# Performance work log

Measured on AMD Instinct MI355X. Metric: run time of the kernel, lower is better.

The kernel has to match this reference:

```python
import jax, jax.numpy as jnp
import numpy as np

EMBED_DIM = 1024
NUM_HEADS = 16
HEAD_DIM = EMBED_DIM // NUM_HEADS
ROPE_BASE = 10000.0


def _rope_cos_sin(seq_len, dim, dtype=jnp.float32):
    inv_freq = 1.0 / (ROPE_BASE ** (jnp.arange(0, dim, 2, dtype=jnp.float32) / dim))
    pos = jnp.arange(seq_len, dtype=jnp.float32)
    freqs = jnp.outer(pos, inv_freq)              # [S, dim/2]
    emb = jnp.concatenate([freqs, freqs], axis=-1)  # [S, dim]
    return jnp.cos(emb).astype(dtype), jnp.sin(emb).astype(dtype)


def _rotate_half(x):
    half = x.shape[-1] // 2
    return jnp.concatenate([-x[..., half:], x[..., :half]], axis=-1)


def setup_inputs() -> dict:
    key = jax.random.key(0)
    ks = jax.random.split(key, 12)
    B, S, E = 4, 2048, EMBED_DIM
    std = 1.0 / np.sqrt(E)
    inp = {
        'query': jax.random.normal(ks[0], (B, S, E), jnp.float32),
        'key': jax.random.normal(ks[1], (B, S, E), jnp.float32),
        'value': jax.random.normal(ks[2], (B, S, E), jnp.float32),
        'Wq': jax.random.uniform(ks[3], (E, E), jnp.float32, -std, std),
        'bq': jax.random.uniform(ks[4], (E,), jnp.float32, -std, std),
        'Wk': jax.random.uniform(ks[5], (E, E), jnp.float32, -std, std),
        'bk': jax.random.uniform(ks[6], (E,), jnp.float32, -std, std),
        'Wv': jax.random.uniform(ks[7], (E, E), jnp.float32, -std, std),
        'bv': jax.random.uniform(ks[8], (E,), jnp.float32, -std, std),
        'Wo': jax.random.uniform(ks[9], (E, E), jnp.float32, -std, std),
        'bo': jax.random.uniform(ks[10], (E,), jnp.float32, -std, std),
    }
    return inp


def reference(query, key, value, Wq, bq, Wk, bk, Wv, bv, Wo, bo):
    B, Sq, E = query.shape
    Sk = key.shape[1]
    H, D = NUM_HEADS, HEAD_DIM
    scale = D ** -0.5

    q = query @ Wq.T + bq
    k = key @ Wk.T + bk
    v = value @ Wv.T + bv

    # [B, H, S, D]
    q = q.reshape(B, Sq, H, D).transpose(0, 2, 1, 3)
    k = k.reshape(B, Sk, H, D).transpose(0, 2, 1, 3)
    v = v.reshape(B, Sk, H, D).transpose(0, 2, 1, 3)

    cos, sin = _rope_cos_sin(Sq, D, q.dtype)  # [S, D]; module slices by seq_len_q for both
    cos = cos[None, None]  # [1,1,S,D]
    sin = sin[None, None]
    q = q * cos + _rotate_half(q) * sin
    k = k * cos + _rotate_half(k) * sin

    scores = jnp.einsum('bhqd,bhkd->bhqk', q, k) * scale
    attn = jax.nn.softmax(scores, axis=-1)  # dropout p=0.0 -> identity
    out = jnp.einsum('bhqk,bhkd->bhqd', attn, v)
    out = out.transpose(0, 2, 1, 3).reshape(B, Sq, E)
    out = out @ Wo.T + bo
    attn_avg = attn.mean(axis=1)  # [B, Sq, Sk]
    return out, attn_avg
```

## Files before the change

kernel.cpp:

```cpp
#include <hip/hip_runtime.h>
#include <math.h>

#define TB 4
#define TS 2048
#define TE 1024
#define TH 16
#define TD 64
#define TM_ (TB*TS)

#define WS_Q   0
#define WS_K   8388608
#define WS_L   16777216
#define WS_TAB 16908288

typedef __attribute__((ext_vector_type(8))) short bf16x8;
typedef __attribute__((ext_vector_type(4))) float f32x4;

static __device__ inline unsigned fbits(float x) {
    union { float f; unsigned u; } v; v.f = x; return v.u;
}
static __device__ inline float bits2f(unsigned u) {
    union { unsigned u; float f; } v; v.u = u; return v.f;
}
static __device__ inline unsigned pack_rhu(float a, float b) {
    return __builtin_amdgcn_perm(fbits(b) + 0x8000u, fbits(a) + 0x8000u, 0x07060302u);
}
static __device__ inline void split2(float x0, float x1, unsigned& hp, unsigned& lp) {
    unsigned u0 = fbits(x0) + 0x8000u, u1 = fbits(x1) + 0x8000u;
    hp = __builtin_amdgcn_perm(u1, u0, 0x07060302u);
    float h0 = bits2f(u0 & 0xffff0000u);
    float h1 = bits2f(u1 & 0xffff0000u);
    lp = pack_rhu(x0 - h0, x1 - h1);
}

template<int MODE>
__global__ __launch_bounds__(256, 2)
void gemm_nt(const float* __restrict__ X, const float* __restrict__ W,
             const float* __restrict__ bias, float* __restrict__ out)
{
    __shared__ short Ah[128][40], Al[128][40];
    __shared__ short Bh[128][40], Bl[128][40];

    const int tid  = threadIdx.x;
    const int lane = tid & 63;
    const int wv   = tid >> 6;
    const int t16  = lane & 15;
    const int quad = lane >> 4;
    const int wm   = (wv >> 1) * 64;
    const int wn   = (wv & 1) * 64;
    const int m0 = blockIdx.y * 128;
    const int n0 = blockIdx.x * 128;
    const int K = TE, N = TE;

    const int srow = tid >> 1;
    const int skc  = (tid & 1) * 16;
    const float* Xp = X + (size_t)(m0 + srow) * K + skc;
    const float* Wp = W + (size_t)(n0 + srow) * K + skc;

    f32x4 acc[4][4];
    #pragma unroll
    for (int i = 0; i < 4; ++i)
        #pragma unroll
        for (int j = 0; j < 4; ++j) acc[i][j] = (f32x4){0.f, 0.f, 0.f, 0.f};

    for (int kt = 0; kt < K; kt += 32) {
        __syncthreads();
        {
            const float* xp = Xp + kt;
            float4 x0 = *(const float4*)(xp);
            float4 x1 = *(const float4*)(xp + 4);
            float4 x2 = *(const float4*)(xp + 8);
            float4 x3 = *(const float4*)(xp + 12);
            const float* wp = Wp + kt;
            float4 w0 = *(const float4*)(wp);
            float4 w1 = *(const float4*)(wp + 4);
            float4 w2 = *(const float4*)(wp + 8);
            float4 w3 = *(const float4*)(wp + 12);

            unsigned H[8], L[8];
            split2(x0.x, x0.y, H[0], L[0]);
            split2(x0.z, x0.w, H[1], L[1]);
            split2(x1.x, x1.y, H[2], L[2]);
            split2(x1.z, x1.w, H[3], L[3]);
            split2(x2.x, x2.y, H[4], L[4]);
            split2(x2.z, x2.w, H[5], L[5]);
            split2(x3.x, x3.y, H[6], L[6]);
            split2(x3.z, x3.w, H[7], L[7]);
            *(uint4*)&Ah[srow][skc]     = make_uint4(H[0], H[1], H[2], H[3]);
            *(uint4*)&Ah[srow][skc + 8] = make_uint4(H[4], H[5], H[6], H[7]);
            *(uint4*)&Al[srow][skc]     = make_uint4(L[0], L[1], L[2], L[3]);
            *(uint4*)&Al[srow][skc + 8] = make_uint4(L[4], L[5], L[6], L[7]);

            split2(w0.x, w0.y, H[0], L[0]);
            split2(w0.z, w0.w, H[1], L[1]);
            split2(w1.x, w1.y, H[2], L[2]);
            split2(w1.z, w1.w, H[3], L[3]);
            split2(w2.x, w2.y, H[4], L[4]);
            split2(w2.z, w2.w, H[5], L[5]);
            split2(w3.x, w3.y, H[6], L[6]);
            split2(w3.z, w3.w, H[7], L[7]);
            *(uint4*)&Bh[srow][skc]     = make_uint4(H[0], H[1], H[2], H[3]);
            *(uint4*)&Bh[srow][skc + 8] = make_uint4(H[4], H[5], H[6], H[7]);
            *(uint4*)&Bl[srow][skc]     = make_uint4(L[0], L[1], L[2], L[3]);
            *(uint4*)&Bl[srow][skc + 8] = make_uint4(L[4], L[5], L[6], L[7]);
        }
        __syncthreads();

        bf16x8 ah[4], al[4], bh[4], bl[4];
        #pragma unroll
        for (int i = 0; i < 4; ++i) {
            ah[i] = *(const bf16x8*)&Ah[wm + i * 16 + t16][quad * 8];
            al[i] = *(const bf16x8*)&Al[wm + i * 16 + t16][quad * 8];
            bh[i] = *(const bf16x8*)&Bh[wn + i * 16 + t16][quad * 8];
            bl[i] = *(const bf16x8*)&Bl[wn + i * 16 + t16][quad * 8];
        }
        #pragma unroll
        for (int i = 0; i < 4; ++i)
            #pragma unroll
            for (int j = 0; j < 4; ++j) {
                acc[i][j] = __builtin_amdgcn_mfma_f32_16x16x32_bf16(ah[i], bh[j], acc[i][j], 0, 0, 0);
                acc[i][j] = __builtin_amdgcn_mfma_f32_16x16x32_bf16(al[i], bh[j], acc[i][j], 0, 0, 0);
                acc[i][j] = __builtin_amdgcn_mfma_f32_16x16x32_bf16(ah[i], bl[j], acc[i][j], 0, 0, 0);
            }
    }

    if (MODE == 2) {
        short* o16 = (short*)out;
        const int b = m0 >> 11;
        const int sbase0 = (m0 & 2047) + wm + quad * 4;
        #pragma unroll
        for (int j = 0; j < 4; ++j) {
            const int n = n0 + wn + j * 16 + t16;
            const int h = n >> 6, d = n & 63;
            const float bv = bias[n];
            const size_t base = ((size_t)(b * TH + h) * TD + d) * TS;
            #pragma unroll
            for (int i = 0; i < 4; ++i) {
                const int s = sbase0 + i * 16;
                uint2 p = make_uint2(pack_rhu(acc[i][j][0] + bv, acc[i][j][1] + bv),
                                     pack_rhu(acc[i][j][2] + bv, acc[i][j][3] + bv));
                *(uint2*)(o16 + base + s) = p;
            }
        }
        return;
    }

    #pragma unroll
    for (int j = 0; j < 4; ++j) {
        const int n = n0 + wn + j * 16 + t16;
        const float bv = bias[n];
        if (MODE == 0) {
            #pragma unroll
            for (int i = 0; i < 4; ++i)
                #pragma unroll
                for (int r = 0; r < 4; ++r) {
                    const int m = m0 + wm + i * 16 + quad * 4 + r;
                    out[(size_t)m * N + n] = acc[i][j][r] + bv;
                }
        } else {
            const int h = n >> 6, d = n & 63;
            #pragma unroll
            for (int i = 0; i < 4; ++i)
                #pragma unroll
                for (int r = 0; r < 4; ++r) {
                    const int m = m0 + wm + i * 16 + quad * 4 + r;
                    const int bb_ = m >> 11, s = m & 2047;
                    out[((size_t)(bb_ * TH + h) * TS + s) * TD + d] = acc[i][j][r] + bv;
                }
        }
    }
}

__global__ void rope_table(float* __restrict__ tab)
{
    const int idx = blockIdx.x * 256 + threadIdx.x;
    const int d = idx & 31, s = idx >> 5;
    const float e = (float)(2 * d) / 64.0f;
    const float inv = 1.0f / powf(10000.0f, e);
    const float a = (float)s * inv;
    tab[2 * idx + 0] = cosf(a);
    tab[2 * idx + 1] = sinf(a);
}

__global__ void rope_apply(float* __restrict__ Q, float* __restrict__ Kv,
                           const float* __restrict__ tab)
{
    const int idx = blockIdx.x * 256 + threadIdx.x;
    const int half = TB * TH * TS * 32;
    float* P = (idx < half) ? Q : Kv;
    const int u = idx & (half - 1);
    const int d = u & 31;
    const int s = (u >> 5) & 2047;
    const int bh = u >> 16;
    const size_t base = (size_t)bh * (TS * TD) + (size_t)s * TD;
    const float c  = tab[2 * (s * 32 + d) + 0];
    const float sn = tab[2 * (s * 32 + d) + 1];
    const float x0 = P[base + d], x1 = P[base + d + 32];
    P[base + d]      = x0 * c - x1 * sn;
    P[base + d + 32] = x1 * c + x0 * sn;
}

__global__ __launch_bounds__(512, 4)
void attn_flash(const float* __restrict__ Q, const float* __restrict__ Kg,
                const short* __restrict__ VT, float* __restrict__ O,
                float* __restrict__ Ls)
{
    __shared__ short Kh[64][72], Kl[64][72];
    __shared__ short Vt[64][72];
    __shared__ short Ps[128][72];

    const int tid  = threadIdx.x;
    const int lane = tid & 63;
    const int wv   = tid >> 6;
    const int t16  = lane & 15;
    const int quad = lane >> 4;
    const int q0w  = wv * 16;

    const int q0 = blockIdx.x * 128;
    const int h = blockIdx.y, b = blockIdx.z;
    const int bh = b * TH + h;
    const size_t hoff = (size_t)bh * TS * TD;
    const float* Kr = Kg + hoff;
    const short* Vth = VT + (size_t)bh * TD * TS;

    const float qsc = 0.125f * 1.44269504f;
    bf16x8 qfh[2], qfl[2];
    {
        const float* qp = Q + hoff + (size_t)(q0 + q0w + t16) * TD;
        #pragma unroll
        for (int ks = 0; ks < 2; ++ks) {
            float4 a = *(const float4*)(qp + ks * 32 + quad * 8);
            float4 c = *(const float4*)(qp + ks * 32 + quad * 8 + 4);
            union { unsigned u[4]; bf16x8 v; } H, L;
            split2(a.x * qsc, a.y * qsc, H.u[0], L.u[0]);
            split2(a.z * qsc, a.w * qsc, H.u[1], L.u[1]);
            split2(c.x * qsc, c.y * qsc, H.u[2], L.u[2]);
            split2(c.z * qsc, c.w * qsc, H.u[3], L.u[3]);
            qfh[ks] = H.v; qfl[ks] = L.v;
        }
    }

    float lsum[4];
    f32x4 o_acc[4];
    #pragma unroll
    for (int r = 0; r < 4; ++r) lsum[r] = 0.f;
    #pragma unroll
    for (int dt = 0; dt < 4; ++dt) o_acc[dt] = (f32x4){0.f, 0.f, 0.f, 0.f};

    const int krow = tid >> 3;
    const int kcol = (tid & 7) * 8;

    for (int j0 = 0; j0 < TS; j0 += 64) {
        __syncthreads();
        {
            const float* kp = Kr + (size_t)(j0 + krow) * TD + kcol;
            float4 a = *(const float4*)kp;
            float4 c = *(const float4*)(kp + 4);
            union { unsigned u[4]; } H, L;
            split2(a.x, a.y, H.u[0], L.u[0]);
            split2(a.z, a.w, H.u[1], L.u[1]);
            split2(c.x, c.y, H.u[2], L.u[2]);
            split2(c.z, c.w, H.u[3], L.u[3]);
            *(uint4*)&Kh[krow][kcol] = make_uint4(H.u[0], H.u[1], H.u[2], H.u[3]);
            *(uint4*)&Kl[krow][kcol] = make_uint4(L.u[0], L.u[1], L.u[2], L.u[3]);
            uint4 vv = *(const uint4*)(Vth + (size_t)krow * TS + j0 + kcol);
            *(uint4*)&Vt[krow][kcol] = vv;
        }
        __syncthreads();

        f32x4 sc[4];
        #pragma unroll
        for (int t = 0; t < 4; ++t) sc[t] = (f32x4){0.f, 0.f, 0.f, 0.f};
        #pragma unroll
        for (int t = 0; t < 4; ++t) {
            #pragma unroll
            for (int ks = 0; ks < 2; ++ks) {
                bf16x8 kf_h = *(const bf16x8*)&Kh[t * 16 + t16][ks * 32 + quad * 8];
                bf16x8 kf_l = *(const bf16x8*)&Kl[t * 16 + t16][ks * 32 + quad * 8];
                sc[t] = __builtin_amdgcn_mfma_f32_16x16x32_bf16(qfh[ks], kf_h, sc[t], 0, 0, 0);
                sc[t] = __builtin_amdgcn_mfma_f32_16x16x32_bf16(qfh[ks], kf_l, sc[t], 0, 0, 0);
                sc[t] = __builtin_amdgcn_mfma_f32_16x16x32_bf16(qfl[ks], kf_h, sc[t], 0, 0, 0);
            }
        }

        #pragma unroll
        for (int t = 0; t < 4; ++t) {
            float p0 = __builtin_amdgcn_exp2f(sc[t][0]);
            float p1 = __builtin_amdgcn_exp2f(sc[t][1]);
            float p2 = __builtin_amdgcn_exp2f(sc[t][2]);
            float p3 = __builtin_amdgcn_exp2f(sc[t][3]);
            lsum[0] += p0; lsum[1] += p1; lsum[2] += p2; lsum[3] += p3;
            const int col = t * 16 + t16;
            Ps[q0w + quad * 4 + 0][col] = (short)(pack_rhu(p0, p0) & 0xffff);
            Ps[q0w + quad * 4 + 1][col] = (short)(pack_rhu(p1, p1) & 0xffff);
            Ps[q0w + quad * 4 + 2][col] = (short)(pack_rhu(p2, p2) & 0xffff);
            Ps[q0w + quad * 4 + 3][col] = (short)(pack_rhu(p3, p3) & 0xffff);
        }

        #pragma unroll
        for (int ks = 0; ks < 2; ++ks) {
            bf16x8 pa = *(const bf16x8*)&Ps[q0w + t16][ks * 32 + quad * 8];
            #pragma unroll
            for (int dt = 0; dt < 4; ++dt) {
                bf16x8 vb = *(const bf16x8*)&Vt[dt * 16 + t16][ks * 32 + quad * 8];
                o_acc[dt] = __builtin_amdgcn_mfma_f32_16x16x32_bf16(pa, vb, o_acc[dt], 0, 0, 0);
            }
        }
    }

    #pragma unroll
    for (int r = 0; r < 4; ++r) {
        #pragma unroll
        for (int off = 1; off < 16; off <<= 1)
            lsum[r] += __shfl_xor(lsum[r], off, 16);
    }

    #pragma unroll
    for (int r = 0; r < 4; ++r) {
        const int row = q0 + q0w + quad * 4 + r;
        const float inv = 1.0f / lsum[r];
        #pragma unroll
        for (int dt = 0; dt < 4; ++dt)
            O[((size_t)(b * TS) + row) * TE + h * TD + dt * 16 + t16] = o_acc[dt][r] * inv;
        if (t16 == 0)
            Ls[(size_t)bh * TS + row] = lsum[r];
    }
}

__global__ __launch_bounds__(256, 2)
void attn_avg_k(const float* __restrict__ Q, const float* __restrict__ Kg,
                const float* __restrict__ Ls, float* __restrict__ AV)
{
    __shared__ short Qt[128][72];
    __shared__ short Kt[128][72];
    __shared__ float ML[TH][128];

    const int tid  = threadIdx.x;
    const int lane = tid & 63;
    const int wv   = tid >> 6;
    const int t16  = lane & 15;
    const int quad = lane >> 4;
    const int wq = (wv >> 1) * 64;
    const int wj = (wv & 1) * 64;

    const int j0 = blockIdx.x * 128;
    const int q0 = blockIdx.y * 128;
    const int b  = blockIdx.z;

    #pragma unroll
    for (int i = 0; i < 8; ++i) {
        const int u = tid + 256 * i;
        const int h = u >> 7, r = u & 127;
        ML[h][r] = 1.0f / Ls[(size_t)(b * TH + h) * TS + q0 + r];
    }

    f32x4 acc[4][4];
    #pragma unroll
    for (int mt = 0; mt < 4; ++mt)
        #pragma unroll
        for (int nt = 0; nt < 4; ++nt) acc[mt][nt] = (f32x4){0.f, 0.f, 0.f, 0.f};

    const float qscale = 0.125f * 1.44269504f;

    for (int h = 0; h < TH; ++h) {
        __syncthreads();
        const size_t hoff = (size_t)(b * TH + h) * TS * TD;
        #pragma unroll
        for (int i = 0; i < 8; ++i) {
            const int f = tid + 256 * i;
            const int row = f >> 4;
            const int dq = (f & 15) * 4;
            float4 qv = *(const float4*)(Q + hoff + (size_t)(q0 + row) * TD + dq);
            uint2 qp = make_uint2(pack_rhu(qv.x * qscale, qv.y * qscale),
                                  pack_rhu(qv.z * qscale, qv.w * qscale));
            *(uint2*)&Qt[row][dq] = qp;
            float4 kv = *(const float4*)(Kg + hoff + (size_t)(j0 + row) * TD + dq);
            uint2 kp = make_uint2(pack_rhu(kv.x, kv.y), pack_rhu(kv.z, kv.w));
            *(uint2*)&Kt[row][dq] = kp;
        }
        __syncthreads();

        f32x4 sc[4][4];
        #pragma unroll
        for (int mt = 0; mt < 4; ++mt)
            #pragma unroll
            for (int nt = 0; nt < 4; ++nt) sc[mt][nt] = (f32x4){0.f, 0.f, 0.f, 0.f};
        #pragma unroll
        for (int ks = 0; ks < 2; ++ks) {
            bf16x8 af[4], bf[4];
            #pragma unroll
            for (int mt = 0; mt < 4; ++mt)
                af[mt] = *(const bf16x8*)&Qt[wq + mt * 16 + t16][ks * 32 + quad * 8];
            #pragma unroll
            for (int nt = 0; nt < 4; ++nt)
                bf[nt] = *(const bf16x8*)&Kt[wj + nt * 16 + t16][ks * 32 + quad * 8];
            #pragma unroll
            for (int mt = 0; mt < 4; ++mt)
                #pragma unroll
                for (int nt = 0; nt < 4; ++nt)
                    sc[mt][nt] = __builtin_amdgcn_mfma_f32_16x16x32_bf16(af[mt], bf[nt], sc[mt][nt], 0, 0, 0);
        }

        #pragma unroll
        for (int mt = 0; mt < 4; ++mt) {
            const int rl = wq + mt * 16 + quad * 4;
            const float lv[4] = {ML[h][rl], ML[h][rl + 1], ML[h][rl + 2], ML[h][rl + 3]};
            #pragma unroll
            for (int nt = 0; nt < 4; ++nt)
                #pragma unroll
                for (int r = 0; r < 4; ++r)
                    acc[mt][nt][r] = fmaf(__builtin_amdgcn_exp2f(sc[mt][nt][r]), lv[r], acc[mt][nt][r]);
        }
    }

    const float inv_h = 1.0f / (float)TH;
    #pragma unroll
    for (int mt = 0; mt < 4; ++mt) {
        #pragma unroll
        for (int r = 0; r < 4; ++r) {
            const int row = q0 + wq + mt * 16 + quad * 4 + r;
            #pragma unroll
            for (int nt = 0; nt < 4; ++nt) {
                const int col = j0 + wj + nt * 16 + t16;
                AV[((size_t)b * TS + row) * TS + col] = acc[mt][nt][r] * inv_h;
            }
        }
    }
}

extern "C" void kernel_launch(void* const* d_in, const int* in_sizes, int n_in,
                              void* d_out, int out_size, void* d_ws, size_t ws_size,
                              hipStream_t stream)
{
    const float* query = (const float*)d_in[0];
    const float* key   = (const float*)d_in[1];
    const float* value = (const float*)d_in[2];
    const float* Wq = (const float*)d_in[3];
    const float* bq = (const float*)d_in[4];
    const float* Wk = (const float*)d_in[5];
    const float* bk = (const float*)d_in[6];
    const float* Wv = (const float*)d_in[7];
    const float* bv = (const float*)d_in[8];
    const float* Wo = (const float*)d_in[9];
    const float* bo = (const float*)d_in[10];

    float* ws  = (float*)d_ws;
    float* Qr  = ws + WS_Q;
    float* Kr  = ws + WS_K;
    float* Lsf = ws + WS_L;
    float* tab = ws + WS_TAB;

    float* out  = (float*)d_out;
    float* attn = out + (size_t)TB * TS * TE;
    short* VT = (short*)attn;
    float* Ow = attn + 4194304;

    dim3 blk(256);
    dim3 gproj(TE / 128, TM_ / 128);

    gemm_nt<1><<<gproj, blk, 0, stream>>>(query, Wq, bq, Qr);
    gemm_nt<1><<<gproj, blk, 0, stream>>>(key,   Wk, bk, Kr);
    gemm_nt<2><<<gproj, blk, 0, stream>>>(value, Wv, bv, (float*)VT);
    rope_table<<<dim3(256), blk, 0, stream>>>(tab);
    rope_apply<<<dim3(32768), blk, 0, stream>>>(Qr, Kr, tab);
    attn_flash<<<dim3(TS / 128, TH, TB), dim3(512), 0, stream>>>(Qr, Kr, VT, Ow, Lsf);
    gemm_nt<0><<<gproj, blk, 0, stream>>>(Ow, Wo, bo, out);
    attn_avg_k<<<dim3(TS / 128, TS / 128, TB), blk, 0, stream>>>(Qr, Kr, Lsf, attn);
}
```

Measured before the change: 716.3 us.

## Pre-split inputs into swizzled bf16 hi/lo layouts shared across GEMMs and attention

Adds a split_rows pass that converts activations and weights into XOR-swizzled bf16 hi/lo arrays in global memory, so the projection GEMMs load ready-made bf16 tiles instead of converting fp32 in every block. RoPE is fused with Q scaling and the hi/lo split, so attention and the attn-average kernel read compact swizzled bf16 Q/K directly. The V and O layouts change to swizzled tiles, flash attention emits split O for the output GEMM, and attention occupancy is raised. In exchange there are extra passes over global memory and more kernel launches, plus workspace aliasing inside the output buffer.

```diff
diff --git a/kernel.cpp b/kernel.cpp
--- a/kernel.cpp
+++ b/kernel.cpp
@@ -25,7 +25,10 @@
 static __device__ inline unsigned pack_rhu(float a, float b) {
     return __builtin_amdgcn_perm(fbits(b) + 0x8000u, fbits(a) + 0x8000u, 0x07060302u);
 }
-static __device__ inline void split2(float x0, float x1, unsigned& hp, unsigned& lp) {
+static __device__ inline short bf16s(float x) {
+    return (short)((fbits(x) + 0x8000u) >> 16);
+}
+static __device__ inline void split2r(float x0, float x1, unsigned& hp, unsigned& lp) {
     unsigned u0 = fbits(x0) + 0x8000u, u1 = fbits(x1) + 0x8000u;
     hp = __builtin_amdgcn_perm(u1, u0, 0x07060302u);
     float h0 = bits2f(u0 & 0xffff0000u);
@@ -33,13 +36,36 @@
     lp = pack_rhu(x0 - h0, x1 - h1);
 }
 
+__global__ __launch_bounds__(256, 4)
+void split_rows(const float* __restrict__ src, unsigned* __restrict__ dst)
+{
+    const int idx = blockIdx.x * 256 + threadIdx.x;
+    const int kt  = idx & 15;
+    const int row = idx >> 4;
+    const uint4* sp = (const uint4*)(src + (size_t)row * 1024 + kt * 64);
+    unsigned* dp = dst + (size_t)row * 1024 + kt * 32;
+    const int key = row & 7;
+    #pragma unroll
+    for (int ch = 0; ch < 8; ++ch) {
+        uint4 v0 = sp[ch * 2 + 0];
+        uint4 v1 = sp[ch * 2 + 1];
+        unsigned h[4], l[4];
+        split2r(bits2f(v0.x), bits2f(v0.y), h[0], l[0]);
+        split2r(bits2f(v0.z), bits2f(v0.w), h[1], l[1]);
+        split2r(bits2f(v1.x), bits2f(v1.y), h[2], l[2]);
+        split2r(bits2f(v1.z), bits2f(v1.w), h[3], l[3]);
+        const int slot = ch ^ key;
+        *(uint4*)(dp + slot * 4)       = make_uint4(h[0], h[1], h[2], h[3]);
+        *(uint4*)(dp + 512 + slot * 4) = make_uint4(l[0], l[1], l[2], l[3]);
+    }
+}
+
 template<int MODE>
 __global__ __launch_bounds__(256, 2)
-void gemm_nt(const float* __restrict__ X, const float* __restrict__ W,
-             const float* __restrict__ bias, float* __restrict__ out)
-{
-    __shared__ short Ah[128][40], Al[128][40];
-    __shared__ short Bh[128][40], Bl[128][40];
+void gemm3(const unsigned* __restrict__ X2, const unsigned* __restrict__ W2,
+           const float* __restrict__ bias, float* __restrict__ out)
+{
+    __shared__ short Ah[128 * 64], Al[128 * 64], Bh[128 * 64], Bl[128 * 64];
 
     const int tid  = threadIdx.x;
     const int lane = tid & 63;
@@ -50,12 +76,9 @@
     const int wn   = (wv & 1) * 64;
     const int m0 = blockIdx.y * 128;
     const int n0 = blockIdx.x * 128;
-    const int K = TE, N = TE;
-
-    const int srow = tid >> 1;
-    const int skc  = (tid & 1) * 16;
-    const float* Xp = X + (size_t)(m0 + srow) * K + skc;
-    const float* Wp = W + (size_t)(n0 + srow) * K + skc;
+
+    const int cx0 = ((quad) ^ (t16 & 7)) * 8;
+    const int cx1 = ((4 + quad) ^ (t16 & 7)) * 8;
 
     f32x4 acc[4][4];
     #pragma unroll
@@ -63,83 +86,65 @@
         #pragma unroll
         for (int j = 0; j < 4; ++j) acc[i][j] = (f32x4){0.f, 0.f, 0.f, 0.f};
 
-    for (int kt = 0; kt < K; kt += 32) {
+    int srow[4], ssl[4];
+    #pragma unroll
+    for (int i = 0; i < 4; ++i) {
+        const int p = i * 256 + tid;
+        srow[i] = p >> 3;
+        ssl[i]  = (p ^ (p >> 3)) & 7;
+    }
+
+    for (int kt = 0; kt < 16; ++kt) {
         __syncthreads();
-        {
-            const float* xp = Xp + kt;
-            float4 x0 = *(const float4*)(xp);
-            float4 x1 = *(const float4*)(xp + 4);
-            float4 x2 = *(const float4*)(xp + 8);
-            float4 x3 = *(const float4*)(xp + 12);
-            const float* wp = Wp + kt;
-            float4 w0 = *(const float4*)(wp);
-            float4 w1 = *(const float4*)(wp + 4);
-            float4 w2 = *(const float4*)(wp + 8);
-            float4 w3 = *(const float4*)(wp + 12);
-
-            unsigned H[8], L[8];
-            split2(x0.x, x0.y, H[0], L[0]);
-            split2(x0.z, x0.w, H[1], L[1]);
-            split2(x1.x, x1.y, H[2], L[2]);
-            split2(x1.z, x1.w, H[3], L[3]);
-            split2(x2.x, x2.y, H[4], L[4]);
-            split2(x2.z, x2.w, H[5], L[5]);
-            split2(x3.x, x3.y, H[6], L[6]);
-            split2(x3.z, x3.w, H[7], L[7]);
-            *(uint4*)&Ah[srow][skc]     = make_uint4(H[0], H[1], H[2], H[3]);
-            *(uint4*)&Ah[srow][skc + 8] = make_uint4(H[4], H[5], H[6], H[7]);
-            *(uint4*)&Al[srow][skc]     = make_uint4(L[0], L[1], L[2], L[3]);
-            *(uint4*)&Al[srow][skc + 8] = make_uint4(L[4], L[5], L[6], L[7]);
-
-            split2(w0.x, w0.y, H[0], L[0]);
-            split2(w0.z, w0.w, H[1], L[1]);
-            split2(w1.x, w1.y, H[2], L[2]);
-            split2(w1.z, w1.w, H[3], L[3]);
-            split2(w2.x, w2.y, H[4], L[4]);
-            split2(w2.z, w2.w, H[5], L[5]);
-            split2(w3.x, w3.y, H[6], L[6]);
-            split2(w3.z, w3.w, H[7], L[7]);
-            *(uint4*)&Bh[srow][skc]     = make_uint4(H[0], H[1], H[2], H[3]);
-            *(uint4*)&Bh[srow][skc + 8] = make_uint4(H[4], H[5], H[6], H[7]);
-            *(uint4*)&Bl[srow][skc]     = make_uint4(L[0], L[1], L[2], L[3]);
-            *(uint4*)&Bl[srow][skc + 8] = make_uint4(L[4], L[5], L[6], L[7]);
+        #pragma unroll
+        for (int i = 0; i < 4; ++i) {
+            const size_t xa = (size_t)(m0 + srow[i]) * 1024 + kt * 32 + ssl[i] * 4;
+            *(uint4*)&Ah[srow[i] * 64 + ssl[i] * 8] = *(const uint4*)(X2 + xa);
+            *(uint4*)&Al[srow[i] * 64 + ssl[i] * 8] = *(const uint4*)(X2 + xa + 512);
+            const size_t wa = (size_t)(n0 + srow[i]) * 1024 + kt * 32 + ssl[i] * 4;
+            *(uint4*)&Bh[srow[i] * 64 + ssl[i] * 8] = *(const uint4*)(W2 + wa);
+            *(uint4*)&Bl[srow[i] * 64 + ssl[i] * 8] = *(const uint4*)(W2 + wa + 512);
         }
         __syncthreads();
-
-        bf16x8 ah[4], al[4], bh[4], bl[4];
-        #pragma unroll
-        for (int i = 0; i < 4; ++i) {
-            ah[i] = *(const bf16x8*)&Ah[wm + i * 16 + t16][quad * 8];
-            al[i] = *(const bf16x8*)&Al[wm + i * 16 + t16][quad * 8];
-            bh[i] = *(const bf16x8*)&Bh[wn + i * 16 + t16][quad * 8];
-            bl[i] = *(const bf16x8*)&Bl[wn + i * 16 + t16][quad * 8];
-        }
-        #pragma unroll
-        for (int i = 0; i < 4; ++i)
-            #pragma unroll
-            for (int j = 0; j < 4; ++j) {
-                acc[i][j] = __builtin_amdgcn_mfma_f32_16x16x32_bf16(ah[i], bh[j], acc[i][j], 0, 0, 0);
-                acc[i][j] = __builtin_amdgcn_mfma_f32_16x16x32_bf16(al[i], bh[j], acc[i][j], 0, 0, 0);
-                acc[i][j] = __builtin_amdgcn_mfma_f32_16x16x32_bf16(ah[i], bl[j], acc[i][j], 0, 0, 0);
+        #pragma unroll
+        for (int ks = 0; ks < 2; ++ks) {
+            const int cx = ks ? cx1 : cx0;
+            bf16x8 ah[4], al[4], bh[4], bl[4];
+            #pragma unroll
+            for (int i = 0; i < 4; ++i) {
+                ah[i] = *(const bf16x8*)&Ah[(wm + i * 16 + t16) * 64 + cx];
+                al[i] = *(const bf16x8*)&Al[(wm + i * 16 + t16) * 64 + cx];
+                bh[i] = *(const bf16x8*)&Bh[(wn + i * 16 + t16) * 64 + cx];
+                bl[i] = *(const bf16x8*)&Bl[(wn + i * 16 + t16) * 64 + cx];
             }
+            #pragma unroll
+            for (int i = 0; i < 4; ++i)
+                #pragma unroll
+                for (int j = 0; j < 4; ++j) {
+                    acc[i][j] = __builtin_amdgcn_mfma_f32_16x16x32_bf16(ah[i], bh[j], acc[i][j], 0, 0, 0);
+                    acc[i][j] = __builtin_amdgcn_mfma_f32_16x16x32_bf16(al[i], bh[j], acc[i][j], 0, 0, 0);
+                    acc[i][j] = __builtin_amdgcn_mfma_f32_16x16x32_bf16(ah[i], bl[j], acc[i][j], 0, 0, 0);
+                }
+        }
     }
 
     if (MODE == 2) {
         short* o16 = (short*)out;
         const int b = m0 >> 11;
-        const int sbase0 = (m0 & 2047) + wm + quad * 4;
+        const int stile = ((m0 & 2047) + wm) >> 6;
         #pragma unroll
         for (int j = 0; j < 4; ++j) {
             const int n = n0 + wn + j * 16 + t16;
             const int h = n >> 6, d = n & 63;
             const float bv = bias[n];
-            const size_t base = ((size_t)(b * TH + h) * TD + d) * TS;
+            const size_t dbase = (((size_t)(b * TH + h) * 32 + stile) * 64 + d) * 64;
             #pragma unroll
             for (int i = 0; i < 4; ++i) {
-                const int s = sbase0 + i * 16;
+                const int chunk = 2 * i + (quad >> 1);
+                const int slot = chunk ^ (d & 7);
                 uint2 p = make_uint2(pack_rhu(acc[i][j][0] + bv, acc[i][j][1] + bv),
                                      pack_rhu(acc[i][j][2] + bv, acc[i][j][3] + bv));
-                *(uint2*)(o16 + base + s) = p;
+                *(uint2*)(o16 + dbase + slot * 8 + (quad & 1) * 4) = p;
             }
         }
         return;
@@ -155,7 +160,7 @@
                 #pragma unroll
                 for (int r = 0; r < 4; ++r) {
                     const int m = m0 + wm + i * 16 + quad * 4 + r;
-                    out[(size_t)m * N + n] = acc[i][j][r] + bv;
+                    out[(size_t)m * TE + n] = acc[i][j][r] + bv;
                 }
         } else {
             const int h = n >> 6, d = n & 63;
@@ -182,32 +187,53 @@
     tab[2 * idx + 1] = sinf(a);
 }
 
-__global__ void rope_apply(float* __restrict__ Q, float* __restrict__ Kv,
-                           const float* __restrict__ tab)
+__global__ __launch_bounds__(256, 2)
+void rope_split(float* __restrict__ Q, float* __restrict__ Kv,
+                const float* __restrict__ tab)
 {
     const int idx = blockIdx.x * 256 + threadIdx.x;
-    const int half = TB * TH * TS * 32;
-    float* P = (idx < half) ? Q : Kv;
-    const int u = idx & (half - 1);
-    const int d = u & 31;
-    const int s = (u >> 5) & 2047;
-    const int bh = u >> 16;
-    const size_t base = (size_t)bh * (TS * TD) + (size_t)s * TD;
-    const float c  = tab[2 * (s * 32 + d) + 0];
-    const float sn = tab[2 * (s * 32 + d) + 1];
-    const float x0 = P[base + d], x1 = P[base + d + 32];
-    P[base + d]      = x0 * c - x1 * sn;
-    P[base + d + 32] = x1 * c + x0 * sn;
-}
-
-__global__ __launch_bounds__(512, 4)
-void attn_flash(const float* __restrict__ Q, const float* __restrict__ Kg,
-                const short* __restrict__ VT, float* __restrict__ O,
+    const int s  = idx & 2047;
+    const int bh = (idx >> 11) & 63;
+    const int qk = idx >> 17;
+    float* P = qk ? Kv : Q;
+    const float scale = qk ? 1.0f : (0.125f * 1.44269504f);
+    unsigned* rp = (unsigned*)(P + ((size_t)bh * TS + s) * 64);
+
+    unsigned xu[64];
+    #pragma unroll
+    for (int i = 0; i < 16; ++i) {
+        uint4 v = *(const uint4*)(rp + i * 4);
+        xu[4 * i + 0] = v.x; xu[4 * i + 1] = v.y;
+        xu[4 * i + 2] = v.z; xu[4 * i + 3] = v.w;
+    }
+    const float* tb = tab + (size_t)s * 64;
+    #pragma unroll
+    for (int d = 0; d < 32; ++d) {
+        const float c = tb[2 * d], sn = tb[2 * d + 1];
+        const float x0 = bits2f(xu[d]), x1 = bits2f(xu[d + 32]);
+        xu[d]      = fbits((x0 * c - x1 * sn) * scale);
+        xu[d + 32] = fbits((x1 * c + x0 * sn) * scale);
+    }
+    const int key = s & 7;
+    #pragma unroll
+    for (int ch = 0; ch < 8; ++ch) {
+        unsigned h[4], l[4];
+        #pragma unroll
+        for (int p = 0; p < 4; ++p)
+            split2r(bits2f(xu[ch * 8 + 2 * p]), bits2f(xu[ch * 8 + 2 * p + 1]), h[p], l[p]);
+        const int slot = ch ^ key;
+        *(uint4*)(rp + slot * 4)      = make_uint4(h[0], h[1], h[2], h[3]);
+        *(uint4*)(rp + 32 + slot * 4) = make_uint4(l[0], l[1], l[2], l[3]);
+    }
+}
+
+__global__ __launch_bounds__(512, 6)
+void attn_flash(const short* __restrict__ Qs, const short* __restrict__ Ks,
+                const short* __restrict__ VT, short* __restrict__ O,
                 float* __restrict__ Ls)
 {
-    __shared__ short Kh[64][72], Kl[64][72];
-    __shared__ short Vt[64][72];
-    __shared__ short Ps[128][72];
+    __shared__ short KhL[4096], KlL[4096], VtL[4096];
+    __shared__ short PsL[8192];
 
     const int tid  = threadIdx.x;
     const int lane = tid & 63;
@@ -219,52 +245,36 @@
     const int q0 = blockIdx.x * 128;
     const int h = blockIdx.y, b = blockIdx.z;
     const int bh = b * TH + h;
-    const size_t hoff = (size_t)bh * TS * TD;
-    const float* Kr = Kg + hoff;
-    const short* Vth = VT + (size_t)bh * TD * TS;
-
-    const float qsc = 0.125f * 1.44269504f;
+
+    const int cx0 = ((quad) ^ (t16 & 7)) * 8;
+    const int cx1 = ((4 + quad) ^ (t16 & 7)) * 8;
+
     bf16x8 qfh[2], qfl[2];
     {
-        const float* qp = Q + hoff + (size_t)(q0 + q0w + t16) * TD;
-        #pragma unroll
-        for (int ks = 0; ks < 2; ++ks) {
-            float4 a = *(const float4*)(qp + ks * 32 + quad * 8);
-            float4 c = *(const float4*)(qp + ks * 32 + quad * 8 + 4);
-            union { unsigned u[4]; bf16x8 v; } H, L;
-            split2(a.x * qsc, a.y * qsc, H.u[0], L.u[0]);
-            split2(a.z * qsc, a.w * qsc, H.u[1], L.u[1]);
-            split2(c.x * qsc, c.y * qsc, H.u[2], L.u[2]);
-            split2(c.z * qsc, c.w * qsc, H.u[3], L.u[3]);
-            qfh[ks] = H.v; qfl[ks] = L.v;
-        }
-    }
-
-    float lsum[4];
+        const short* qrow = Qs + ((size_t)bh * TS + q0 + q0w + t16) * 128;
+        qfh[0] = *(const bf16x8*)(qrow + cx0);
+        qfh[1] = *(const bf16x8*)(qrow + cx1);
+        qfl[0] = *(const bf16x8*)(qrow + 64 + cx0);
+        qfl[1] = *(const bf16x8*)(qrow + 64 + cx1);
+    }
+
+    float lsum[4] = {0.f, 0.f, 0.f, 0.f};
     f32x4 o_acc[4];
     #pragma unroll
-    for (int r = 0; r < 4; ++r) lsum[r] = 0.f;
-    #pragma unroll
     for (int dt = 0; dt < 4; ++dt) o_acc[dt] = (f32x4){0.f, 0.f, 0.f, 0.f};
 
-    const int krow = tid >> 3;
-    const int kcol = (tid & 7) * 8;
+    const int srow = tid >> 3;
+    const int ssl  = (tid ^ srow) & 7;
+    const short* kbase = Ks + (size_t)bh * TS * 128;
+    const short* vbase = VT + (size_t)bh * 131072;
 
     for (int j0 = 0; j0 < TS; j0 += 64) {
         __syncthreads();
         {
-            const float* kp = Kr + (size_t)(j0 + krow) * TD + kcol;
-            float4 a = *(const float4*)kp;
-            float4 c = *(const float4*)(kp + 4);
-            union { unsigned u[4]; } H, L;
-            split2(a.x, a.y, H.u[0], L.u[0]);
-            split2(a.z, a.w, H.u[1], L.u[1]);
-            split2(c.x, c.y, H.u[2], L.u[2]);
-            split2(c.z, c.w, H.u[3], L.u[3]);
-            *(uint4*)&Kh[krow][kcol] = make_uint4(H.u[0], H.u[1], H.u[2], H.u[3]);
-            *(uint4*)&Kl[krow][kcol] = make_uint4(L.u[0], L.u[1], L.u[2], L.u[3]);
-            uint4 vv = *(const uint4*)(Vth + (size_t)krow * TS + j0 + kcol);
-            *(uint4*)&Vt[krow][kcol] = vv;
+            const short* krow = kbase + (size_t)(j0 + srow) * 128;
+            *(uint4*)&KhL[srow * 64 + ssl * 8] = *(const uint4*)(krow + ssl * 8);
+            *(uint4*)&KlL[srow * 64 + ssl * 8] = *(const uint4*)(krow + 64 + ssl * 8);
+            *(uint4*)&VtL[tid * 8] = *(const uint4*)(vbase + (j0 << 6) + tid * 8);
         }
         __syncthreads();
 
@@ -273,14 +283,17 @@
         for (int t = 0; t < 4; ++t) sc[t] = (f32x4){0.f, 0.f, 0.f, 0.f};
         #pragma unroll
         for (int t = 0; t < 4; ++t) {
-            #pragma unroll
-            for (int ks = 0; ks < 2; ++ks) {
-                bf16x8 kf_h = *(const bf16x8*)&Kh[t * 16 + t16][ks * 32 + quad * 8];
-                bf16x8 kf_l = *(const bf16x8*)&Kl[t * 16 + t16][ks * 32 + quad * 8];
-                sc[t] = __builtin_amdgcn_mfma_f32_16x16x32_bf16(qfh[ks], kf_h, sc[t], 0, 0, 0);
-                sc[t] = __builtin_amdgcn_mfma_f32_16x16x32_bf16(qfh[ks], kf_l, sc[t], 0, 0, 0);
-                sc[t] = __builtin_amdgcn_mfma_f32_16x16x32_bf16(qfl[ks], kf_h, sc[t], 0, 0, 0);
-            }
+            const int rb = (t * 16 + t16) * 64;
+            bf16x8 kh0 = *(const bf16x8*)&KhL[rb + cx0];
+            bf16x8 kl0 = *(const bf16x8*)&KlL[rb + cx0];
+            sc[t] = __builtin_amdgcn_mfma_f32_16x16x32_bf16(qfh[0], kh0, sc[t], 0, 0, 0);
+            sc[t] = __builtin_amdgcn_mfma_f32_16x16x32_bf16(qfh[0], kl0, sc[t], 0, 0, 0);
+            sc[t] = __builtin_amdgcn_mfma_f32_16x16x32_bf16(qfl[0], kh0, sc[t], 0, 0, 0);
+            bf16x8 kh1 = *(const bf16x8*)&KhL[rb + cx1];
+            bf16x8 kl1 = *(const bf16x8*)&KlL[rb + cx1];
+            sc[t] = __builtin_amdgcn_mfma_f32_16x16x32_bf16(qfh[1], kh1, sc[t], 0, 0, 0);
+            sc[t] = __builtin_amdgcn_mfma_f32_16x16x32_bf16(qfh[1], kl1, sc[t], 0, 0, 0);
+            sc[t] = __builtin_amdgcn_mfma_f32_16x16x32_bf16(qfl[1], kh1, sc[t], 0, 0, 0);
         }
 
         #pragma unroll
@@ -290,20 +303,27 @@
             float p2 = __builtin_amdgcn_exp2f(sc[t][2]);
             float p3 = __builtin_amdgcn_exp2f(sc[t][3]);
             lsum[0] += p0; lsum[1] += p1; lsum[2] += p2; lsum[3] += p3;
-            const int col = t * 16 + t16;
-            Ps[q0w + quad * 4 + 0][col] = (short)(pack_rhu(p0, p0) & 0xffff);
-            Ps[q0w + quad * 4 + 1][col] = (short)(pack_rhu(p1, p1) & 0xffff);
-            Ps[q0w + quad * 4 + 2][col] = (short)(pack_rhu(p2, p2) & 0xffff);
-            Ps[q0w + quad * 4 + 3][col] = (short)(pack_rhu(p3, p3) & 0xffff);
-        }
-
-        #pragma unroll
-        for (int ks = 0; ks < 2; ++ks) {
-            bf16x8 pa = *(const bf16x8*)&Ps[q0w + t16][ks * 32 + quad * 8];
+            const int cb = 2 * t + (t16 >> 3);
+            const int co = t16 & 7;
+            PsL[(q0w + quad * 4 + 0) * 64 + ((cb ^ ((quad * 4 + 0) & 7)) * 8) + co] = bf16s(p0);
+            PsL[(q0w + quad * 4 + 1) * 64 + ((cb ^ ((quad * 4 + 1) & 7)) * 8) + co] = bf16s(p1);
+            PsL[(q0w + quad * 4 + 2) * 64 + ((cb ^ ((quad * 4 + 2) & 7)) * 8) + co] = bf16s(p2);
+            PsL[(q0w + quad * 4 + 3) * 64 + ((cb ^ ((quad * 4 + 3) & 7)) * 8) + co] = bf16s(p3);
+        }
+
+        {
+            const int pr = (q0w + t16) * 64;
+            bf16x8 pa0 = *(const bf16x8*)&PsL[pr + cx0];
             #pragma unroll
             for (int dt = 0; dt < 4; ++dt) {
-                bf16x8 vb = *(const bf16x8*)&Vt[dt * 16 + t16][ks * 32 + quad * 8];
-                o_acc[dt] = __builtin_amdgcn_mfma_f32_16x16x32_bf16(pa, vb, o_acc[dt], 0, 0, 0);
+                bf16x8 vb = *(const bf16x8*)&VtL[(dt * 16 + t16) * 64 + cx0];
+                o_acc[dt] = __builtin_amdgcn_mfma_f32_16x16x32_bf16(pa0, vb, o_acc[dt], 0, 0, 0);
+            }
+            bf16x8 pa1 = *(const bf16x8*)&PsL[pr + cx1];
+            #pragma unroll
+            for (int dt = 0; dt < 4; ++dt) {
+                bf16x8 vb = *(const bf16x8*)&VtL[(dt * 16 + t16) * 64 + cx1];
+                o_acc[dt] = __builtin_amdgcn_mfma_f32_16x16x32_bf16(pa1, vb, o_acc[dt], 0, 0, 0);
             }
         }
     }
@@ -319,20 +339,27 @@
     for (int r = 0; r < 4; ++r) {
         const int row = q0 + q0w + quad * 4 + r;
         const float inv = 1.0f / lsum[r];
-        #pragma unroll
-        for (int dt = 0; dt < 4; ++dt)
-            O[((size_t)(b * TS) + row) * TE + h * TD + dt * 16 + t16] = o_acc[dt][r] * inv;
+        short* orow = O + ((size_t)b * TS + row) * 2048;
+        const int key = (quad * 4 + r) & 7;
+        #pragma unroll
+        for (int dt = 0; dt < 4; ++dt) {
+            const float val = o_acc[dt][r] * inv;
+            const int ch = 2 * dt + (t16 >> 3);
+            const int pos = h * 64 + ((ch ^ key) * 8) + (t16 & 7);
+            const unsigned hb = (fbits(val) + 0x8000u) & 0xffff0000u;
+            orow[pos] = (short)(hb >> 16);
+            orow[1024 + pos] = bf16s(val - bits2f(hb));
+        }
         if (t16 == 0)
             Ls[(size_t)bh * TS + row] = lsum[r];
     }
 }
 
 __global__ __launch_bounds__(256, 2)
-void attn_avg_k(const float* __restrict__ Q, const float* __restrict__ Kg,
+void attn_avg_k(const short* __restrict__ Qs, const short* __restrict__ Ks,
                 const float* __restrict__ Ls, float* __restrict__ AV)
 {
-    __shared__ short Qt[128][72];
-    __shared__ short Kt[128][72];
+    __shared__ short Qt[8192], Kt[8192];
     __shared__ float ML[TH][128];
 
     const int tid  = threadIdx.x;
@@ -347,6 +374,9 @@
     const int q0 = blockIdx.y * 128;
     const int b  = blockIdx.z;
 
+    const int cx0 = ((quad) ^ (t16 & 7)) * 8;
+    const int cx1 = ((4 + quad) ^ (t16 & 7)) * 8;
+
     #pragma unroll
     for (int i = 0; i < 8; ++i) {
         const int u = tid + 256 * i;
@@ -360,23 +390,17 @@
         #pragma unroll
         for (int nt = 0; nt < 4; ++nt) acc[mt][nt] = (f32x4){0.f, 0.f, 0.f, 0.f};
 
-    const float qscale = 0.125f * 1.44269504f;
-
     for (int h = 0; h < TH; ++h) {
         __syncthreads();
-        const size_t hoff = (size_t)(b * TH + h) * TS * TD;
-        #pragma unroll
-        for (int i = 0; i < 8; ++i) {
-            const int f = tid + 256 * i;
-            const int row = f >> 4;
-            const int dq = (f & 15) * 4;
-            float4 qv = *(const float4*)(Q + hoff + (size_t)(q0 + row) * TD + dq);
-            uint2 qp = make_uint2(pack_rhu(qv.x * qscale, qv.y * qscale),
-                                  pack_rhu(qv.z * qscale, qv.w * qscale));
-            *(uint2*)&Qt[row][dq] = qp;
-            float4 kv = *(const float4*)(Kg + hoff + (size_t)(j0 + row) * TD + dq);
-            uint2 kp = make_uint2(pack_rhu(kv.x, kv.y), pack_rhu(kv.z, kv.w));
-            *(uint2*)&Kt[row][dq] = kp;
+        const size_t rbq = (size_t)(b * TH + h) * TS + q0;
+        const size_t rbk = (size_t)(b * TH + h) * TS + j0;
+        #pragma unroll
+        for (int i = 0; i < 4; ++i) {
+            const int p = i * 256 + tid;
+            const int row = p >> 3;
+            const int sl = (p ^ row) & 7;
+            *(uint4*)&Qt[row * 64 + sl * 8] = *(const uint4*)(Qs + (rbq + row) * 128 + sl * 8);
+            *(uint4*)&Kt[row * 64 + sl * 8] = *(const uint4*)(Ks + (rbk + row) * 128 + sl * 8);
         }
         __syncthreads();
 
@@ -387,13 +411,14 @@
             for (int nt = 0; nt < 4; ++nt) sc[mt][nt] = (f32x4){0.f, 0.f, 0.f, 0.f};
         #pragma unroll
         for (int ks = 0; ks < 2; ++ks) {
+            const int cx = ks ? cx1 : cx0;
             bf16x8 af[4], bf[4];
             #pragma unroll
             for (int mt = 0; mt < 4; ++mt)
-                af[mt] = *(const bf16x8*)&Qt[wq + mt * 16 + t16][ks * 32 + quad * 8];
+                af[mt] = *(const bf16x8*)&Qt[(wq + mt * 16 + t16) * 64 + cx];
             #pragma unroll
             for (int nt = 0; nt < 4; ++nt)
-                bf[nt] = *(const bf16x8*)&Kt[wj + nt * 16 + t16][ks * 32 + quad * 8];
+                bf[nt] = *(const bf16x8*)&Kt[(wj + nt * 16 + t16) * 64 + cx];
             #pragma unroll
             for (int mt = 0; mt < 4; ++mt)
                 #pragma unroll
@@ -452,18 +477,37 @@
 
     float* out  = (float*)d_out;
     float* attn = out + (size_t)TB * TS * TE;
-    short* VT = (short*)attn;
-    float* Ow = attn + 4194304;
+    short*    VTs  = (short*)attn;
+    unsigned* WspO = (unsigned*)attn;
+    unsigned* Xsp  = (unsigned*)(attn + 4194304);
+    short*    Osp  = (short*)(attn + 4194304);
+    unsigned* Wsp  = (unsigned*)(attn + 12582912);
 
     dim3 blk(256);
     dim3 gproj(TE / 128, TM_ / 128);
 
-    gemm_nt<1><<<gproj, blk, 0, stream>>>(query, Wq, bq, Qr);
-    gemm_nt<1><<<gproj, blk, 0, stream>>>(key,   Wk, bk, Kr);
-    gemm_nt<2><<<gproj, blk, 0, stream>>>(value, Wv, bv, (float*)VT);
     rope_table<<<dim3(256), blk, 0, stream>>>(tab);
-    rope_apply<<<dim3(32768), blk, 0, stream>>>(Qr, Kr, tab);
-    attn_flash<<<dim3(TS / 128, TH, TB), dim3(512), 0, stream>>>(Qr, Kr, VT, Ow, Lsf);
-    gemm_nt<0><<<gproj, blk, 0, stream>>>(Ow, Wo, bo, out);
-    attn_avg_k<<<dim3(TS / 128, TS / 128, TB), blk, 0, stream>>>(Qr, Kr, Lsf, attn);
-}
+
+    split_rows<<<dim3(512), blk, 0, stream>>>(query, Xsp);
+    split_rows<<<dim3(64),  blk, 0, stream>>>(Wq, Wsp);
+    gemm3<1><<<gproj, blk, 0, stream>>>(Xsp, Wsp, bq, Qr);
+
+    split_rows<<<dim3(512), blk, 0, stream>>>(key, Xsp);
+    split_rows<<<dim3(64),  blk, 0, stream>>>(Wk, Wsp);
+    gemm3<1><<<gproj, blk, 0, stream>>>(Xsp, Wsp, bk, Kr);
+
+    split_rows<<<dim3(512), blk, 0, stream>>>(value, Xsp);
+    split_rows<<<dim3(64),  blk, 0, stream>>>(Wv, Wsp);
+    gemm3<2><<<gproj, blk, 0, stream>>>(Xsp, Wsp, bv, (float*)VTs);
+
+    rope_split<<<dim3(1024), blk, 0, stream>>>(Qr, Kr, tab);
+
+    attn_flash<<<dim3(TS / 128, TH, TB), dim3(512), 0, stream>>>(
+        (const short*)Qr, (const short*)Kr, VTs, Osp, Lsf);
+
+    split_rows<<<dim3(64), blk, 0, stream>>>(Wo, WspO);
+    gemm3<0><<<gproj, blk, 0, stream>>>((const unsigned*)Osp, WspO, bo, out);
+
+    attn_avg_k<<<dim3(TS / 128, TS / 128, TB), blk, 0, stream>>>(
+        (const short*)Qr, (const short*)Kr, Lsf, attn);
+}
```

After: 906.4 us. 26.5% more time.

## Swizzle attention LDS tiles with XOR layout and remap blocks for XCD locality

Applied to the files above, without the earlier changes.

Replaces the padded 72-wide shared-memory tiles for K, V and P in the flash attention kernel with unpadded 64-wide tiles addressed through an XOR swizzle of 8-element chunks. This is meant to avoid LDS bank conflicts while shrinking LDS usage. It also remaps the linear block index so that blocks sharing the same batch and head land on the same XCD, which should improve L2 reuse of K and V. The added index arithmetic is a small cost, and the P writes remain scalar short stores.

```diff
diff --git a/kernel.cpp b/kernel.cpp
--- a/kernel.cpp
+++ b/kernel.cpp
@@ -24,6 +24,9 @@
 }
 static __device__ inline unsigned pack_rhu(float a, float b) {
     return __builtin_amdgcn_perm(fbits(b) + 0x8000u, fbits(a) + 0x8000u, 0x07060302u);
+}
+static __device__ inline short bf16s(float x) {
+    return (short)((fbits(x) + 0x8000u) >> 16);
 }
 static __device__ inline void split2(float x0, float x1, unsigned& hp, unsigned& lp) {
     unsigned u0 = fbits(x0) + 0x8000u, u1 = fbits(x1) + 0x8000u;
@@ -205,9 +208,9 @@
                 const short* __restrict__ VT, float* __restrict__ O,
                 float* __restrict__ Ls)
 {
-    __shared__ short Kh[64][72], Kl[64][72];
-    __shared__ short Vt[64][72];
-    __shared__ short Ps[128][72];
+    __shared__ short KhL[4096], KlL[4096];
+    __shared__ short VtL[4096];
+    __shared__ short PsL[8192];
 
     const int tid  = threadIdx.x;
     const int lane = tid & 63;
@@ -216,13 +219,23 @@
     const int quad = lane >> 4;
     const int q0w  = wv * 16;
 
-    const int q0 = blockIdx.x * 128;
-    const int h = blockIdx.y, b = blockIdx.z;
+    const int L   = blockIdx.x + 16 * blockIdx.y + 256 * blockIdx.z;
+    const int xcd = L & 7;
+    const int i_  = L >> 3;
+    const int qt  = i_ & 15;
+    const int g   = (xcd << 3) | (i_ >> 4);
+    const int h   = g & 15;
+    const int b   = g >> 4;
+
+    const int q0 = qt * 128;
     const int bh = b * TH + h;
     const size_t hoff = (size_t)bh * TS * TD;
     const float* Kr = Kg + hoff;
     const short* Vth = VT + (size_t)bh * TD * TS;
 
+    const int cx0 = ((quad) ^ (t16 & 7)) * 8;
+    const int cx1 = ((4 + quad) ^ (t16 & 7)) * 8;
+
     const float qsc = 0.125f * 1.44269504f;
     bf16x8 qfh[2], qfl[2];
     {
@@ -231,40 +244,39 @@
         for (int ks = 0; ks < 2; ++ks) {
             float4 a = *(const float4*)(qp + ks * 32 + quad * 8);
             float4 c = *(const float4*)(qp + ks * 32 + quad * 8 + 4);
-            union { unsigned u[4]; bf16x8 v; } H, L;
-            split2(a.x * qsc, a.y * qsc, H.u[0], L.u[0]);
-            split2(a.z * qsc, a.w * qsc, H.u[1], L.u[1]);
-            split2(c.x * qsc, c.y * qsc, H.u[2], L.u[2]);
-            split2(c.z * qsc, c.w * qsc, H.u[3], L.u[3]);
-            qfh[ks] = H.v; qfl[ks] = L.v;
-        }
-    }
-
-    float lsum[4];
+            union { unsigned u[4]; bf16x8 v; } H, Lo;
+            split2(a.x * qsc, a.y * qsc, H.u[0], Lo.u[0]);
+            split2(a.z * qsc, a.w * qsc, H.u[1], Lo.u[1]);
+            split2(c.x * qsc, c.y * qsc, H.u[2], Lo.u[2]);
+            split2(c.z * qsc, c.w * qsc, H.u[3], Lo.u[3]);
+            qfh[ks] = H.v; qfl[ks] = Lo.v;
+        }
+    }
+
+    float lsum[4] = {0.f, 0.f, 0.f, 0.f};
     f32x4 o_acc[4];
     #pragma unroll
-    for (int r = 0; r < 4; ++r) lsum[r] = 0.f;
-    #pragma unroll
     for (int dt = 0; dt < 4; ++dt) o_acc[dt] = (f32x4){0.f, 0.f, 0.f, 0.f};
 
     const int krow = tid >> 3;
-    const int kcol = (tid & 7) * 8;
+    const int kch  = tid & 7;
+    const int ksl  = (kch ^ (krow & 7)) * 8;
 
     for (int j0 = 0; j0 < TS; j0 += 64) {
         __syncthreads();
         {
-            const float* kp = Kr + (size_t)(j0 + krow) * TD + kcol;
+            const float* kp = Kr + (size_t)(j0 + krow) * TD + kch * 8;
             float4 a = *(const float4*)kp;
             float4 c = *(const float4*)(kp + 4);
-            union { unsigned u[4]; } H, L;
-            split2(a.x, a.y, H.u[0], L.u[0]);
-            split2(a.z, a.w, H.u[1], L.u[1]);
-            split2(c.x, c.y, H.u[2], L.u[2]);
-            split2(c.z, c.w, H.u[3], L.u[3]);
-            *(uint4*)&Kh[krow][kcol] = make_uint4(H.u[0], H.u[1], H.u[2], H.u[3]);
-            *(uint4*)&Kl[krow][kcol] = make_uint4(L.u[0], L.u[1], L.u[2], L.u[3]);
-            uint4 vv = *(const uint4*)(Vth + (size_t)krow * TS + j0 + kcol);
-            *(uint4*)&Vt[krow][kcol] = vv;
+            unsigned H[4], Lo[4];
+            split2(a.x, a.y, H[0], Lo[0]);
+            split2(a.z, a.w, H[1], Lo[1]);
+            split2(c.x, c.y, H[2], Lo[2]);
+            split2(c.z, c.w, H[3], Lo[3]);
+            *(uint4*)&KhL[krow * 64 + ksl] = make_uint4(H[0], H[1], H[2], H[3]);
+            *(uint4*)&KlL[krow * 64 + ksl] = make_uint4(Lo[0], Lo[1], Lo[2], Lo[3]);
+            uint4 vv = *(const uint4*)(Vth + (size_t)krow * TS + j0 + kch * 8);
+            *(uint4*)&VtL[krow * 64 + ksl] = vv;
         }
         __syncthreads();
 
@@ -273,14 +285,17 @@
         for (int t = 0; t < 4; ++t) sc[t] = (f32x4){0.f, 0.f, 0.f, 0.f};
         #pragma unroll
         for (int t = 0; t < 4; ++t) {
-            #pragma unroll
-            for (int ks = 0; ks < 2; ++ks) {
-                bf16x8 kf_h = *(const bf16x8*)&Kh[t * 16 + t16][ks * 32 + quad * 8];
-                bf16x8 kf_l = *(const bf16x8*)&Kl[t * 16 + t16][ks * 32 + quad * 8];
-                sc[t] = __builtin_amdgcn_mfma_f32_16x16x32_bf16(qfh[ks], kf_h, sc[t], 0, 0, 0);
-                sc[t] = __builtin_amdgcn_mfma_f32_16x16x32_bf16(qfh[ks], kf_l, sc[t], 0, 0, 0);
-                sc[t] = __builtin_amdgcn_mfma_f32_16x16x32_bf16(qfl[ks], kf_h, sc[t], 0, 0, 0);
-            }
+            const int rb = (t * 16 + t16) * 64;
+            bf16x8 kh0 = *(const bf16x8*)&KhL[rb + cx0];
+            bf16x8 kl0 = *(const bf16x8*)&KlL[rb + cx0];
+            sc[t] = __builtin_amdgcn_mfma_f32_16x16x32_bf16(qfh[0], kh0, sc[t], 0, 0, 0);
+            sc[t] = __builtin_amdgcn_mfma_f32_16x16x32_bf16(qfh[0], kl0, sc[t], 0, 0, 0);
+            sc[t] = __builtin_amdgcn_mfma_f32_16x16x32_bf16(qfl[0], kh0, sc[t], 0, 0, 0);
+            bf16x8 kh1 = *(const bf16x8*)&KhL[rb + cx1];
+            bf16x8 kl1 = *(const bf16x8*)&KlL[rb + cx1];
+            sc[t] = __builtin_amdgcn_mfma_f32_16x16x32_bf16(qfh[1], kh1, sc[t], 0, 0, 0);
+            sc[t] = __builtin_amdgcn_mfma_f32_16x16x32_bf16(qfh[1], kl1, sc[t], 0, 0, 0);
+            sc[t] = __builtin_amdgcn_mfma_f32_16x16x32_bf16(qfl[1], kh1, sc[t], 0, 0, 0);
         }
 
         #pragma unroll
@@ -290,20 +305,28 @@
             float p2 = __builtin_amdgcn_exp2f(sc[t][2]);
             float p3 = __builtin_amdgcn_exp2f(sc[t][3]);
             lsum[0] += p0; lsum[1] += p1; lsum[2] += p2; lsum[3] += p3;
-            const int col = t * 16 + t16;
-            Ps[q0w + quad * 4 + 0][col] = (short)(pack_rhu(p0, p0) & 0xffff);
-            Ps[q0w + quad * 4 + 1][col] = (short)(pack_rhu(p1, p1) & 0xffff);
-            Ps[q0w + quad * 4 + 2][col] = (short)(pack_rhu(p2, p2) & 0xffff);
-            Ps[q0w + quad * 4 + 3][col] = (short)(pack_rhu(p3, p3) & 0xffff);
-        }
-
-        #pragma unroll
-        for (int ks = 0; ks < 2; ++ks) {
-            bf16x8 pa = *(const bf16x8*)&Ps[q0w + t16][ks * 32 + quad * 8];
+            const int cb = 2 * t + (t16 >> 3);
+            const int co = t16 & 7;
+            const int r0 = q0w + quad * 4;
+            PsL[(r0 + 0) * 64 + ((cb ^ ((r0 + 0) & 7)) * 8) + co] = bf16s(p0);
+            PsL[(r0 + 1) * 64 + ((cb ^ ((r0 + 1) & 7)) * 8) + co] = bf16s(p1);
+            PsL[(r0 + 2) * 64 + ((cb ^ ((r0 + 2) & 7)) * 8) + co] = bf16s(p2);
+            PsL[(r0 + 3) * 64 + ((cb ^ ((r0 + 3) & 7)) * 8) + co] = bf16s(p3);
+        }
+
+        {
+            const int pr = (q0w + t16) * 64;
+            bf16x8 pa0 = *(const bf16x8*)&PsL[pr + cx0];
             #pragma unroll
             for (int dt = 0; dt < 4; ++dt) {
-                bf16x8 vb = *(const bf16x8*)&Vt[dt * 16 + t16][ks * 32 + quad * 8];
-                o_acc[dt] = __builtin_amdgcn_mfma_f32_16x16x32_bf16(pa, vb, o_acc[dt], 0, 0, 0);
+                bf16x8 vb = *(const bf16x8*)&VtL[(dt * 16 + t16) * 64 + cx0];
+                o_acc[dt] = __builtin_amdgcn_mfma_f32_16x16x32_bf16(pa0, vb, o_acc[dt], 0, 0, 0);
+            }
+            bf16x8 pa1 = *(const bf16x8*)&PsL[pr + cx1];
+            #pragma unroll
+            for (int dt = 0; dt < 4; ++dt) {
+                bf16x8 vb = *(const bf16x8*)&VtL[(dt * 16 + t16) * 64 + cx1];
+                o_acc[dt] = __builtin_amdgcn_mfma_f32_16x16x32_bf16(pa1, vb, o_acc[dt], 0, 0, 0);
             }
         }
     }
```

Result: faster. 677.3 us (-5.4%).
